# Optimization experiments

Measured on AMD Instinct MI355X. Metric: run time of the kernel, lower is better.

Reference implementation:

```python
import jax, jax.numpy as jnp
import numpy as np

D_MODEL = 2048
NUM_HEADS = 16
HEAD_DIM = D_MODEL // NUM_HEADS
B, T = 4, 2048


def setup_inputs() -> dict:
    key = jax.random.key(0)
    ks = jax.random.split(key, 9)
    s = 1.0 / np.sqrt(D_MODEL)
    inp = {"x": jax.random.normal(ks[0], (B, T, D_MODEL), dtype=jnp.float32)}
    for i, name in enumerate(["q", "k", "v", "o"]):
        inp[f"W{name}"] = jax.random.uniform(ks[1 + 2 * i], (D_MODEL, D_MODEL), minval=-s, maxval=s, dtype=jnp.float32)
        inp[f"b{name}"] = jax.random.uniform(ks[2 + 2 * i], (D_MODEL,), minval=-s, maxval=s, dtype=jnp.float32)
    return inp


def reference(x, Wq, bq, Wk, bk, Wv, bv, Wo, bo):
    Bx, Tx, _ = x.shape
    H, Dh = NUM_HEADS, HEAD_DIM
    # torch Linear: y = x @ W.T + b
    q = (x @ Wq.T + bq).reshape(Bx, Tx, H, Dh).transpose(0, 2, 1, 3)  # [B,H,T,D]
    k = (x @ Wk.T + bk).reshape(Bx, Tx, H, Dh).transpose(0, 2, 1, 3)
    v = (x @ Wv.T + bv).reshape(Bx, Tx, H, Dh).transpose(0, 2, 1, 3)
    scale = 1.0 / np.sqrt(Dh).astype(np.float32)
    scores = jnp.einsum('bhqd,bhkd->bhqk', q, k) * scale  # [B,H,T,T] (no causal mask, as in source)
    attn = jax.nn.softmax(scores, axis=-1)
    out = jnp.einsum('bhqk,bhkd->bhqd', attn, v)  # [B,H,T,D]
    out = out.transpose(0, 2, 1, 3).reshape(Bx, Tx, H * Dh)
    return out @ Wo.T + bo
```

## Files before the change

kernel.cpp:

```cpp
#include <hip/hip_runtime.h>
#include <hip/hip_bf16.h>

typedef __bf16 bf16x8 __attribute__((ext_vector_type(8)));
typedef __bf16 bf16x4 __attribute__((ext_vector_type(4)));
typedef float floatx4 __attribute__((ext_vector_type(4)));

#define MFMA16(a, b, c) __builtin_amdgcn_mfma_f32_16x16x32_bf16((a), (b), (c), 0, 0, 0)

#define GLOAD16(g, l) __builtin_amdgcn_global_load_lds( \
    (const __attribute__((address_space(1))) unsigned int*)(g), \
    (__attribute__((address_space(3))) unsigned int*)(l), 16, 0, 0)

static constexpr int DM = 2048, NH = 16, HD = 128, BATCH = 4, SEQ = 2048;
static constexpr int MROWS = BATCH * SEQ;
static constexpr float SCALE = 0.08838834764831845f;
static constexpr float PMAX = 3.0f;

static constexpr size_t XE = (size_t)MROWS * DM;
static constexpr size_t WE = (size_t)DM * DM;

__global__ __launch_bounds__(256) void cvt_all(
    const float* __restrict__ x, const float* __restrict__ Wq,
    const float* __restrict__ Wk, const float* __restrict__ Wv,
    const float* __restrict__ Wo, __bf16* __restrict__ dst) {
  const size_t total = XE + 4 * WE;
  size_t stride = (size_t)gridDim.x * 256 * 8;
  for (size_t i = ((size_t)blockIdx.x * 256 + threadIdx.x) * 8; i < total; i += stride) {
    const float* src;
    size_t off;
    if (i < XE) { src = x; off = i; }
    else {
      size_t j = i - XE;
      int seg = (int)(j / WE);
      off = j - (size_t)seg * WE;
      src = seg == 0 ? Wq : (seg == 1 ? Wk : (seg == 2 ? Wv : Wo));
    }
    float4 a = *reinterpret_cast<const float4*>(src + off);
    float4 b = *reinterpret_cast<const float4*>(src + off + 4);
    bf16x8 r;
    r[0] = (__bf16)a.x; r[1] = (__bf16)a.y; r[2] = (__bf16)a.z; r[3] = (__bf16)a.w;
    r[4] = (__bf16)b.x; r[5] = (__bf16)b.y; r[6] = (__bf16)b.z; r[7] = (__bf16)b.w;
    *reinterpret_cast<bf16x8*>(dst + i) = r;
  }
}

__device__ __forceinline__ void gemm256_core(
    const __bf16* __restrict__ A, const __bf16* __restrict__ W,
    unsigned short* sA, unsigned short* sB,
    int tm, int tn, floatx4 (&acc)[8][4]) {
  const int tid = threadIdx.x;
  const int wave = tid >> 6, lane = tid & 63;
  const int q = lane >> 4, ml = lane & 15;
  const int wm = wave >> 2, wn = wave & 3;

  const int csrc = (tid & 3) ^ ((tid >> 3) & 3);
  const __bf16* gA = A + (size_t)(tm + (tid >> 2)) * DM + csrc * 8;
  const __bf16* gB = W + (size_t)(tn + (tid >> 2)) * DM + csrc * 8;
  const size_t rstep = (size_t)128 * DM;
  const int ldsW = wave * 512;

  const int fsw = (q ^ ((ml >> 1) & 3)) * 8;
  const int aOff = (wm * 128 + ml) * 32 + fsw;
  const int bOff = (wn * 64 + ml) * 32 + fsw;

#define STAGE256(s_) do { \
    const int _r = ((s_) & 3) * 8192;   \
    const int _k = (s_) * 32;           \
    GLOAD16(gA + _k,         sA + _r + ldsW); \
    GLOAD16(gA + _k + rstep, sA + _r + 4096 + ldsW); \
    GLOAD16(gB + _k,         sB + _r + ldsW); \
    GLOAD16(gB + _k + rstep, sB + _r + 4096 + ldsW); \
  } while (0)

#define GPHASE(p_, vm_, stage_) do { \
    if (stage_) STAGE256((p_) + 3); \
    asm volatile("s_waitcnt vmcnt(%0)" :: "i"(vm_) : "memory"); \
    __builtin_amdgcn_s_barrier(); \
    __builtin_amdgcn_sched_barrier(0); \
    const int regO = ((p_) & 3) * 8192; \
    bf16x8 aF[8], bF[4]; \
    _Pragma("unroll") \
    for (int t = 0; t < 4; ++t) \
      bF[t] = *reinterpret_cast<const bf16x8*>(sB + regO + bOff + t * 512); \
    _Pragma("unroll") \
    for (int t = 0; t < 8; ++t) \
      aF[t] = *reinterpret_cast<const bf16x8*>(sA + regO + aOff + t * 512); \
    __builtin_amdgcn_s_setprio(1); \
    _Pragma("unroll") \
    for (int mt = 0; mt < 8; ++mt) \
      _Pragma("unroll") \
      for (int ct = 0; ct < 4; ++ct) \
        acc[mt][ct] = MFMA16(aF[mt], bF[ct], acc[mt][ct]); \
    __builtin_amdgcn_s_setprio(0); \
    __builtin_amdgcn_s_barrier(); \
  } while (0)

  STAGE256(0); STAGE256(1); STAGE256(2);

#pragma unroll 4
  for (int p = 0; p < 60; ++p) GPHASE(p, 12, 1);
  GPHASE(60, 12, 1);
  GPHASE(61, 8, 0);
  GPHASE(62, 4, 0);
  GPHASE(63, 0, 0);
#undef GPHASE
#undef STAGE256
}

__global__ __launch_bounds__(512, 2) void qkv_gemm256(
    const __bf16* __restrict__ X,
    const __bf16* __restrict__ Wq, const __bf16* __restrict__ Wk,
    const __bf16* __restrict__ Wv,
    const float* __restrict__ bq, const float* __restrict__ bk,
    const float* __restrict__ bv,
    __bf16* __restrict__ qh, __bf16* __restrict__ kh, __bf16* __restrict__ vt) {
  __shared__ unsigned short sA[4 * 256 * 32];
  __shared__ unsigned short sB[4 * 256 * 32];
  const int bx = blockIdx.x;
  const int which = bx >> 3;
  const int tn = (bx & 7) * 256;
  const int tm = blockIdx.y * 256;
  const __bf16* W = which == 0 ? Wq : (which == 1 ? Wk : Wv);
  const float* bias = which == 0 ? bq : (which == 1 ? bk : bv);

  floatx4 acc[8][4] = {};
  gemm256_core(X, W, sA, sB, tm, tn, acc);

  const int tid = threadIdx.x, wave = tid >> 6, lane = tid & 63;
  const int q = lane >> 4, ml = lane & 15;
  const int wm = wave >> 2, wn = wave & 3;

  __syncthreads();

  if (which < 2) {
    unsigned short* reg = (wave < 4) ? sA + wave * 8192 : sB + (wave - 4) * 8192;
#pragma unroll
    for (int ct = 0; ct < 4; ++ct) {
      int n = tn + wn * 64 + ct * 16 + ml;
      float bv_ = bias[n];
#pragma unroll
      for (int mt = 0; mt < 8; ++mt)
#pragma unroll
        for (int r = 0; r < 4; ++r) {
          int row = mt * 16 + q * 4 + r;
          int col = ct * 16 + ml;
          __bf16 pb = (__bf16)(acc[mt][ct][r] + bv_);
          reg[row * 64 + (((col >> 3) ^ ((row >> 1) & 7)) << 3) + (col & 7)] =
              __builtin_bit_cast(unsigned short, pb);
        }
    }
    __bf16* dst = which == 0 ? qh : kh;
    const int rr = lane >> 3, cc = lane & 7;
#pragma unroll
    for (int i = 0; i < 16; ++i) {
      int row = i * 8 + rr;
      int4 v = *reinterpret_cast<const int4*>(
          reg + row * 64 + ((cc ^ ((row >> 1) & 7)) << 3));
      int m = tm + wm * 128 + row;
      int n0 = tn + wn * 64 + cc * 8;
      int b = m >> 11, t = m & 2047, h = n0 >> 7, d = n0 & 127;
      *reinterpret_cast<int4*>(dst + ((size_t)(b * 16 + h) * SEQ + t) * HD + d) = v;
    }
  } else {
#pragma unroll
    for (int ct = 0; ct < 4; ++ct) {
      int n = tn + wn * 64 + ct * 16 + ml;
      float bv_ = bias[n];
      int h = n >> 7, d = n & 127;
#pragma unroll
      for (int mt = 0; mt < 8; ++mt) {
        int m0 = tm + wm * 128 + mt * 16 + q * 4;
        int b = m0 >> 11, t = m0 & 2047;
        bf16x4 pk;
#pragma unroll
        for (int r = 0; r < 4; ++r) pk[r] = (__bf16)(acc[mt][ct][r] + bv_);
        *reinterpret_cast<bf16x4*>(vt + (size_t)((b * 16 + h) * 128 + d) * SEQ + t) = pk;
      }
    }
  }
}

__global__ __launch_bounds__(512, 2) void proj_gemm256(
    const __bf16* __restrict__ A, const __bf16* __restrict__ W,
    const float* __restrict__ bias, float* __restrict__ out) {
  __shared__ unsigned short sA[4 * 256 * 32];
  __shared__ unsigned short sB[4 * 256 * 32];
  const int tn = blockIdx.x * 256;
  const int tm = blockIdx.y * 256;

  floatx4 acc[8][4] = {};
  gemm256_core(A, W, sA, sB, tm, tn, acc);

  const int tid = threadIdx.x, wave = tid >> 6, lane = tid & 63;
  const int q = lane >> 4, ml = lane & 15;
  const int wm = wave >> 2, wn = wave & 3;
#pragma unroll
  for (int ct = 0; ct < 4; ++ct) {
    int n = tn + wn * 64 + ct * 16 + ml;
    float bv_ = bias[n];
#pragma unroll
    for (int mt = 0; mt < 8; ++mt) {
      int m0 = tm + wm * 128 + mt * 16 + q * 4;
#pragma unroll
      for (int r = 0; r < 4; ++r)
        out[(size_t)(m0 + r) * DM + n] = acc[mt][ct][r] + bv_;
    }
  }
}

__global__ __launch_bounds__(512, 4) void mha_attn(
    const __bf16* __restrict__ Q, const __bf16* __restrict__ Kg,
    const __bf16* __restrict__ Vt, __bf16* __restrict__ O) {
  __shared__ unsigned short sK[2][64 * 128];
  __shared__ unsigned short sV[2][128 * 64];
  __shared__ unsigned short sP[128 * 64];

  const int tid = threadIdx.x;
  const int bh = blockIdx.x;
  const int t0 = blockIdx.y * 128;
  const int wave = tid >> 6, lane = tid & 63;
  const int q = lane >> 4, ml = lane & 15;
  const int wrow = wave * 16;

  bf16x8 qf[4];
  {
    const __bf16* qrow = Q + ((size_t)bh * SEQ + t0 + wrow + ml) * HD;
#pragma unroll
    for (int s = 0; s < 4; ++s)
      qf[s] = *reinterpret_cast<const bf16x8*>(qrow + s * 32 + q * 8);
  }

  floatx4 oacc[8] = {};
  float lsum[4] = {0.f, 0.f, 0.f, 0.f};

  const __bf16* kbase = Kg + (size_t)bh * SEQ * HD;
  const __bf16* vbase = Vt + (size_t)bh * HD * SEQ;
  const int lrow4 = lane >> 4, c16 = lane & 15;
  const int lrow8 = lane >> 3, c8 = lane & 7;

#define ASTAGE(slot_, key0_) do { \
    _Pragma("unroll") \
    for (int i = 0; i < 2; ++i) { \
      int kr0 = wave * 8 + i * 4; \
      int kc = c16 ^ ((i * 4 + lrow4) & 7); \
      GLOAD16(kbase + (size_t)((key0_) + kr0 + lrow4) * HD + kc * 8, \
              &sK[slot_][kr0 * 128]); \
      int vr0 = wave * 16 + i * 8; \
      int vc = c8 ^ (lrow8 & 7); \
      GLOAD16(vbase + (size_t)(vr0 + lrow8) * SEQ + (key0_) + vc * 8, \
              &sV[slot_][vr0 * 64]); \
    } } while (0)

#define ACOMPUTE(S_) do { \
    floatx4 sacc[4] = {}; \
    _Pragma("unroll") \
    for (int s = 0; s < 4; ++s) { \
      _Pragma("unroll") \
      for (int ct = 0; ct < 4; ++ct) { \
        bf16x8 kf = *reinterpret_cast<const bf16x8*>( \
            &sK[S_][(ct * 16 + ml) * 128 + (((s * 4 + q) ^ (ml & 7)) * 8)]); \
        sacc[ct] = MFMA16(qf[s], kf, sacc[ct]); \
      } \
    } \
    _Pragma("unroll") \
    for (int ct = 0; ct < 4; ++ct) { \
      _Pragma("unroll") \
      for (int r = 0; r < 4; ++r) { \
        float p = __expf(fmaf(sacc[ct][r], SCALE, -PMAX)); \
        lsum[r] += p; \
        __bf16 pb = (__bf16)p; \
        int lr = wrow + q * 4 + r; \
        int ch = ct * 2 + (ml >> 3); \
        sP[lr * 64 + ((ch ^ (lr & 7)) << 3) + (ml & 7)] = \
            __builtin_bit_cast(unsigned short, pb); \
      } \
    } \
    _Pragma("unroll") \
    for (int s = 0; s < 2; ++s) { \
      int prow = wrow + ml; \
      bf16x8 pf = *reinterpret_cast<const bf16x8*>( \
          &sP[prow * 64 + (((s * 4 + q) ^ (ml & 7)) << 3)]); \
      _Pragma("unroll") \
      for (int ot = 0; ot < 8; ++ot) { \
        bf16x8 vf = *reinterpret_cast<const bf16x8*>( \
            &sV[S_][(ot * 16 + ml) * 64 + (((s * 4 + q) ^ (ml & 7)) * 8)]); \
        oacc[ot] = MFMA16(pf, vf, oacc[ot]); \
      } \
    } } while (0)

  ASTAGE(0, 0);
  for (int kt = 0; kt < 31; ++kt) {
    const int S = kt & 1;
    ASTAGE(S ^ 1, (kt + 1) * 64);
    asm volatile("s_waitcnt vmcnt(4)" ::: "memory");
    __builtin_amdgcn_s_barrier();
    __builtin_amdgcn_sched_barrier(0);
    __builtin_amdgcn_s_setprio(1);
    ACOMPUTE(S);
    __builtin_amdgcn_s_setprio(0);
    asm volatile("" ::: "memory");
    __builtin_amdgcn_s_barrier();
  }
  asm volatile("s_waitcnt vmcnt(0)" ::: "memory");
  __builtin_amdgcn_s_barrier();
  __builtin_amdgcn_sched_barrier(0);
  ACOMPUTE(1);
#undef ACOMPUTE
#undef ASTAGE

#pragma unroll
  for (int r = 0; r < 4; ++r) {
    float s = lsum[r];
    s += __shfl_xor(s, 1); s += __shfl_xor(s, 2);
    s += __shfl_xor(s, 4); s += __shfl_xor(s, 8);
    lsum[r] = 1.0f / s;
  }

  const int b = bh >> 4, h = bh & 15;
  const int rr = lane >> 3, cc = lane & 7;
  __bf16* obase = O + ((size_t)b * SEQ + t0 + wrow) * DM + h * HD;
#pragma unroll
  for (int pass = 0; pass < 2; ++pass) {
    __builtin_amdgcn_sched_barrier(0);
#pragma unroll
    for (int ot = 0; ot < 4; ++ot) {
#pragma unroll
      for (int r = 0; r < 4; ++r) {
        int lr = wrow + q * 4 + r;
        int ch = ot * 2 + (ml >> 3);
        __bf16 ob = (__bf16)(oacc[pass * 4 + ot][r] * lsum[r]);
        sP[lr * 64 + ((ch ^ (lr & 7)) << 3) + (ml & 7)] =
            __builtin_bit_cast(unsigned short, ob);
      }
    }
#pragma unroll
    for (int i = 0; i < 2; ++i) {
      int row16 = i * 8 + rr;
      int gr = wrow + row16;
      int4 v = *reinterpret_cast<const int4*>(
          &sP[gr * 64 + ((cc ^ (gr & 7)) << 3)]);
      *reinterpret_cast<int4*>(obase + (size_t)row16 * DM + pass * 64 + cc * 8) = v;
    }
  }
}

__device__ inline bf16x8 ld8s(const float* p) {
  float4 a = *reinterpret_cast<const float4*>(p);
  float4 b = *reinterpret_cast<const float4*>(p + 4);
  bf16x8 r;
  r[0] = (__bf16)a.x; r[1] = (__bf16)a.y; r[2] = (__bf16)a.z; r[3] = (__bf16)a.w;
  r[4] = (__bf16)b.x; r[5] = (__bf16)b.y; r[6] = (__bf16)b.z; r[7] = (__bf16)b.w;
  return r;
}
__device__ inline bf16x8 ld8s(const __bf16* p) {
  int4 v = *reinterpret_cast<const int4*>(p);
  return __builtin_bit_cast(bf16x8, v);
}

template <typename TA>
__global__ __launch_bounds__(256) void gemm_slow(
    const TA* __restrict__ A, const float* __restrict__ W,
    const float* __restrict__ bias, void* __restrict__ C, int mode, int out_f32) {
  __shared__ unsigned short sA[128 * 72];
  __shared__ unsigned short sW[128 * 72];
  const int tid = threadIdx.x;
  const int tn = blockIdx.x * 128, tm = blockIdx.y * 128;
  const int wave = tid >> 6, lane = tid & 63;
  const int q = lane >> 4, ml = lane & 15;
  const int waveM = (wave >> 1) * 64, waveN = (wave & 1) * 64;
  const int srow = tid >> 3, sc8 = tid & 7;
  floatx4 acc[4][4] = {};
  for (int k0 = 0; k0 < DM; k0 += 64) {
    bf16x8 va[4], vb[4];
#pragma unroll
    for (int i = 0; i < 4; ++i) {
      int row = srow + 32 * i;
      va[i] = ld8s(A + (size_t)(tm + row) * DM + k0 + sc8 * 8);
      vb[i] = ld8s(W + (size_t)(tn + row) * DM + k0 + sc8 * 8);
    }
    __syncthreads();
#pragma unroll
    for (int i = 0; i < 4; ++i) {
      int row = srow + 32 * i;
      *reinterpret_cast<int4*>(&sA[row * 72 + sc8 * 8]) = __builtin_bit_cast(int4, va[i]);
      *reinterpret_cast<int4*>(&sW[row * 72 + sc8 * 8]) = __builtin_bit_cast(int4, vb[i]);
    }
    __syncthreads();
#pragma unroll
    for (int s = 0; s < 2; ++s) {
      bf16x8 aF[4], bF[4];
#pragma unroll
      for (int t = 0; t < 4; ++t)
        aF[t] = *reinterpret_cast<const bf16x8*>(&sA[(waveM + t * 16 + ml) * 72 + s * 32 + q * 8]);
#pragma unroll
      for (int t = 0; t < 4; ++t)
        bF[t] = *reinterpret_cast<const bf16x8*>(&sW[(waveN + t * 16 + ml) * 72 + s * 32 + q * 8]);
#pragma unroll
      for (int rt = 0; rt < 4; ++rt)
#pragma unroll
        for (int ct = 0; ct < 4; ++ct)
          acc[rt][ct] = MFMA16(aF[rt], bF[ct], acc[rt][ct]);
    }
  }
#pragma unroll
  for (int ct = 0; ct < 4; ++ct) {
    int n = tn + waveN + ct * 16 + ml;
    float bv = bias[n];
    int h = n >> 7, d = n & 127;
#pragma unroll
    for (int rt = 0; rt < 4; ++rt) {
      int m0 = tm + waveM + rt * 16 + q * 4;
      int b = m0 >> 11, t = m0 & 2047;
      if (mode == 0) {
        if (out_f32) {
#pragma unroll
          for (int r = 0; r < 4; ++r)
            ((float*)C)[(size_t)(m0 + r) * DM + n] = acc[rt][ct][r] + bv;
        } else {
#pragma unroll
          for (int r = 0; r < 4; ++r)
            ((__bf16*)C)[(size_t)(m0 + r) * DM + n] = (__bf16)(acc[rt][ct][r] + bv);
        }
      } else if (mode == 1) {
        bf16x4 pk;
#pragma unroll
        for (int r = 0; r < 4; ++r) pk[r] = (__bf16)(acc[rt][ct][r] + bv);
        *reinterpret_cast<bf16x4*>((__bf16*)C + (size_t)((b * 16 + h) * 128 + d) * SEQ + t) = pk;
      } else {
#pragma unroll
        for (int r = 0; r < 4; ++r)
          ((__bf16*)C)[((size_t)(b * 16 + h) * SEQ + t + r) * HD + d] =
              (__bf16)(acc[rt][ct][r] + bv);
      }
    }
  }
}

extern "C" void kernel_launch(void* const* d_in, const int* in_sizes, int n_in,
                              void* d_out, int out_size, void* d_ws, size_t ws_size,
                              hipStream_t stream) {
  const float* x  = (const float*)d_in[0];
  const float* Wq = (const float*)d_in[1]; const float* bq = (const float*)d_in[2];
  const float* Wk = (const float*)d_in[3]; const float* bk = (const float*)d_in[4];
  const float* Wv = (const float*)d_in[5]; const float* bv = (const float*)d_in[6];
  const float* Wo = (const float*)d_in[7]; const float* bo = (const float*)d_in[8];

  const size_t needA = 64 + 2 * (4 * XE + 4 * WE);
  dim3 gq(24, 32), gp(8, 32), gs(16, 64), ga(BATCH * NH, SEQ / 128);

  if (ws_size >= needA + 256) {
    __bf16* xc  = (__bf16*)((char*)d_ws + 64);
    __bf16* Wqc = xc + XE;
    __bf16* Wkc = Wqc + WE;
    __bf16* Wvc = Wkc + WE;
    __bf16* Woc = Wvc + WE;
    __bf16* qh  = Woc + WE;
    __bf16* kh  = qh + XE;
    __bf16* vt  = kh + XE;
    __bf16* aw  = xc;

    cvt_all<<<4096, 256, 0, stream>>>(x, Wq, Wk, Wv, Wo, xc);
    qkv_gemm256<<<gq, 512, 0, stream>>>(xc, Wqc, Wkc, Wvc, bq, bk, bv, qh, kh, vt);
    mha_attn<<<ga, 512, 0, stream>>>(qh, kh, vt, aw);
    proj_gemm256<<<gp, 512, 0, stream>>>(aw, Woc, bo, (float*)d_out);
  } else {
    __bf16* qh = (__bf16*)((char*)d_ws + 64);
    __bf16* kh = qh + XE;
    __bf16* vt = kh + XE;
    __bf16* aw = vt + XE;
    gemm_slow<float><<<gs, 256, 0, stream>>>(x, Wq, bq, qh, 2, 0);
    gemm_slow<float><<<gs, 256, 0, stream>>>(x, Wk, bk, kh, 2, 0);
    gemm_slow<float><<<gs, 256, 0, stream>>>(x, Wv, bv, vt, 1, 0);
    mha_attn<<<ga, 512, 0, stream>>>(qh, kh, vt, aw);
    gemm_slow<__bf16><<<gs, 256, 0, stream>>>(aw, Wo, bo, d_out, 0, 1);
  }
}
```

Before: 615.9 us.

## Give each attention wave two 16-row query tiles to reuse K/V fragments

The attention kernel moves from 8 waves of 16 query rows each to 4 waves of 32 query rows each (256 threads per block). Each K and V fragment read from LDS now feeds two MFMAs, which halves LDS read traffic per MFMA. The cooperative staging loop, wait counts and epilogue are rewritten to match the smaller block. In exchange, accumulator registers roughly double (oacc grows to 2x8 floatx4), which may lower occupancy, and each block has fewer waves to hide latency.

```diff
diff --git a/kernel.cpp b/kernel.cpp
--- a/kernel.cpp
+++ b/kernel.cpp
@@ -208,7 +208,7 @@
   }
 }
 
-__global__ __launch_bounds__(512, 4) void mha_attn(
+__global__ __launch_bounds__(256, 2) void mha_attn(
     const __bf16* __restrict__ Q, const __bf16* __restrict__ Kg,
     const __bf16* __restrict__ Vt, __bf16* __restrict__ O) {
   __shared__ unsigned short sK[2][64 * 128];
@@ -220,71 +220,74 @@
   const int t0 = blockIdx.y * 128;
   const int wave = tid >> 6, lane = tid & 63;
   const int q = lane >> 4, ml = lane & 15;
-  const int wrow = wave * 16;
-
-  bf16x8 qf[4];
-  {
-    const __bf16* qrow = Q + ((size_t)bh * SEQ + t0 + wrow + ml) * HD;
+  const int wrow = wave * 32;
+
+  bf16x8 qf[2][4];
+#pragma unroll
+  for (int mt = 0; mt < 2; ++mt) {
+    const __bf16* qrow = Q + ((size_t)bh * SEQ + t0 + wrow + mt * 16 + ml) * HD;
 #pragma unroll
     for (int s = 0; s < 4; ++s)
-      qf[s] = *reinterpret_cast<const bf16x8*>(qrow + s * 32 + q * 8);
-  }
-
-  floatx4 oacc[8] = {};
-  float lsum[4] = {0.f, 0.f, 0.f, 0.f};
+      qf[mt][s] = *reinterpret_cast<const bf16x8*>(qrow + s * 32 + q * 8);
+  }
+
+  floatx4 oacc[2][8] = {};
+  float lsum[2][4] = {};
 
   const __bf16* kbase = Kg + (size_t)bh * SEQ * HD;
   const __bf16* vbase = Vt + (size_t)bh * HD * SEQ;
-  const int lrow4 = lane >> 4, c16 = lane & 15;
-  const int lrow8 = lane >> 3, c8 = lane & 7;
 
 #define ASTAGE(slot_, key0_) do { \
     _Pragma("unroll") \
-    for (int i = 0; i < 2; ++i) { \
-      int kr0 = wave * 8 + i * 4; \
-      int kc = c16 ^ ((i * 4 + lrow4) & 7); \
-      GLOAD16(kbase + (size_t)((key0_) + kr0 + lrow4) * HD + kc * 8, \
-              &sK[slot_][kr0 * 128]); \
-      int vr0 = wave * 16 + i * 8; \
-      int vc = c8 ^ (lrow8 & 7); \
-      GLOAD16(vbase + (size_t)(vr0 + lrow8) * SEQ + (key0_) + vc * 8, \
-              &sV[slot_][vr0 * 64]); \
+    for (int i = 0; i < 4; ++i) { \
+      int krow = i * 16 + (tid >> 4); \
+      int kc = (tid & 15) ^ (krow & 7); \
+      GLOAD16(kbase + (size_t)((key0_) + krow) * HD + kc * 8, \
+              &sK[slot_][i * 2048 + wave * 512]); \
+      int vrow = i * 32 + (tid >> 3); \
+      int vc = (tid & 7) ^ (vrow & 7); \
+      GLOAD16(vbase + (size_t)vrow * SEQ + (key0_) + vc * 8, \
+              &sV[slot_][i * 2048 + wave * 512]); \
     } } while (0)
 
 #define ACOMPUTE(S_) do { \
-    floatx4 sacc[4] = {}; \
+    floatx4 sacc[2][4] = {}; \
     _Pragma("unroll") \
     for (int s = 0; s < 4; ++s) { \
       _Pragma("unroll") \
       for (int ct = 0; ct < 4; ++ct) { \
         bf16x8 kf = *reinterpret_cast<const bf16x8*>( \
             &sK[S_][(ct * 16 + ml) * 128 + (((s * 4 + q) ^ (ml & 7)) * 8)]); \
-        sacc[ct] = MFMA16(qf[s], kf, sacc[ct]); \
+        sacc[0][ct] = MFMA16(qf[0][s], kf, sacc[0][ct]); \
+        sacc[1][ct] = MFMA16(qf[1][s], kf, sacc[1][ct]); \
       } \
     } \
     _Pragma("unroll") \
-    for (int ct = 0; ct < 4; ++ct) { \
+    for (int mt = 0; mt < 2; ++mt) \
       _Pragma("unroll") \
-      for (int r = 0; r < 4; ++r) { \
-        float p = __expf(fmaf(sacc[ct][r], SCALE, -PMAX)); \
-        lsum[r] += p; \
-        __bf16 pb = (__bf16)p; \
-        int lr = wrow + q * 4 + r; \
-        int ch = ct * 2 + (ml >> 3); \
-        sP[lr * 64 + ((ch ^ (lr & 7)) << 3) + (ml & 7)] = \
-            __builtin_bit_cast(unsigned short, pb); \
-      } \
-    } \
+      for (int ct = 0; ct < 4; ++ct) \
+        _Pragma("unroll") \
+        for (int r = 0; r < 4; ++r) { \
+          float p = __expf(fmaf(sacc[mt][ct][r], SCALE, -PMAX)); \
+          lsum[mt][r] += p; \
+          __bf16 pb = (__bf16)p; \
+          int lr = wrow + mt * 16 + q * 4 + r; \
+          int ch = ct * 2 + (ml >> 3); \
+          sP[lr * 64 + ((ch ^ (lr & 7)) << 3) + (ml & 7)] = \
+              __builtin_bit_cast(unsigned short, pb); \
+        } \
     _Pragma("unroll") \
     for (int s = 0; s < 2; ++s) { \
-      int prow = wrow + ml; \
-      bf16x8 pf = *reinterpret_cast<const bf16x8*>( \
-          &sP[prow * 64 + (((s * 4 + q) ^ (ml & 7)) << 3)]); \
+      bf16x8 pf0 = *reinterpret_cast<const bf16x8*>( \
+          &sP[(wrow + ml) * 64 + (((s * 4 + q) ^ (ml & 7)) << 3)]); \
+      bf16x8 pf1 = *reinterpret_cast<const bf16x8*>( \
+          &sP[(wrow + 16 + ml) * 64 + (((s * 4 + q) ^ (ml & 7)) << 3)]); \
       _Pragma("unroll") \
       for (int ot = 0; ot < 8; ++ot) { \
         bf16x8 vf = *reinterpret_cast<const bf16x8*>( \
             &sV[S_][(ot * 16 + ml) * 64 + (((s * 4 + q) ^ (ml & 7)) * 8)]); \
-        oacc[ot] = MFMA16(pf, vf, oacc[ot]); \
+        oacc[0][ot] = MFMA16(pf0, vf, oacc[0][ot]); \
+        oacc[1][ot] = MFMA16(pf1, vf, oacc[1][ot]); \
       } \
     } } while (0)
 
@@ -292,7 +295,7 @@
   for (int kt = 0; kt < 31; ++kt) {
     const int S = kt & 1;
     ASTAGE(S ^ 1, (kt + 1) * 64);
-    asm volatile("s_waitcnt vmcnt(4)" ::: "memory");
+    asm volatile("s_waitcnt vmcnt(8)" ::: "memory");
     __builtin_amdgcn_s_barrier();
     __builtin_amdgcn_sched_barrier(0);
     __builtin_amdgcn_s_setprio(1);
@@ -309,12 +312,14 @@
 #undef ASTAGE
 
 #pragma unroll
-  for (int r = 0; r < 4; ++r) {
-    float s = lsum[r];
-    s += __shfl_xor(s, 1); s += __shfl_xor(s, 2);
-    s += __shfl_xor(s, 4); s += __shfl_xor(s, 8);
-    lsum[r] = 1.0f / s;
-  }
+  for (int mt = 0; mt < 2; ++mt)
+#pragma unroll
+    for (int r = 0; r < 4; ++r) {
+      float s = lsum[mt][r];
+      s += __shfl_xor(s, 1); s += __shfl_xor(s, 2);
+      s += __shfl_xor(s, 4); s += __shfl_xor(s, 8);
+      lsum[mt][r] = 1.0f / s;
+    }
 
   const int b = bh >> 4, h = bh & 15;
   const int rr = lane >> 3, cc = lane & 7;
@@ -323,23 +328,24 @@
   for (int pass = 0; pass < 2; ++pass) {
     __builtin_amdgcn_sched_barrier(0);
 #pragma unroll
-    for (int ot = 0; ot < 4; ++ot) {
-#pragma unroll
-      for (int r = 0; r < 4; ++r) {
-        int lr = wrow + q * 4 + r;
-        int ch = ot * 2 + (ml >> 3);
-        __bf16 ob = (__bf16)(oacc[pass * 4 + ot][r] * lsum[r]);
-        sP[lr * 64 + ((ch ^ (lr & 7)) << 3) + (ml & 7)] =
-            __builtin_bit_cast(unsigned short, ob);
-      }
-    }
-#pragma unroll
-    for (int i = 0; i < 2; ++i) {
-      int row16 = i * 8 + rr;
-      int gr = wrow + row16;
+    for (int mt = 0; mt < 2; ++mt)
+#pragma unroll
+      for (int ot = 0; ot < 4; ++ot)
+#pragma unroll
+        for (int r = 0; r < 4; ++r) {
+          int lr = wrow + mt * 16 + q * 4 + r;
+          int ch = ot * 2 + (ml >> 3);
+          __bf16 ob = (__bf16)(oacc[mt][pass * 4 + ot][r] * lsum[mt][r]);
+          sP[lr * 64 + ((ch ^ (lr & 7)) << 3) + (ml & 7)] =
+              __builtin_bit_cast(unsigned short, ob);
+        }
+#pragma unroll
+    for (int i = 0; i < 4; ++i) {
+      int row32 = i * 8 + rr;
+      int gr = wrow + row32;
       int4 v = *reinterpret_cast<const int4*>(
           &sP[gr * 64 + ((cc ^ (gr & 7)) << 3)]);
-      *reinterpret_cast<int4*>(obase + (size_t)row16 * DM + pass * 64 + cc * 8) = v;
+      *reinterpret_cast<int4*>(obase + (size_t)row32 * DM + pass * 64 + cc * 8) = v;
     }
   }
 }
@@ -461,7 +467,7 @@
 
     cvt_all<<<4096, 256, 0, stream>>>(x, Wq, Wk, Wv, Wo, xc);
     qkv_gemm256<<<gq, 512, 0, stream>>>(xc, Wqc, Wkc, Wvc, bq, bk, bv, qh, kh, vt);
-    mha_attn<<<ga, 512, 0, stream>>>(qh, kh, vt, aw);
+    mha_attn<<<ga, 256, 0, stream>>>(qh, kh, vt, aw);
     proj_gemm256<<<gp, 512, 0, stream>>>(aw, Woc, bo, (float*)d_out);
   } else {
     __bf16* qh = (__bf16*)((char*)d_ws + 64);
@@ -471,7 +477,7 @@
     gemm_slow<float><<<gs, 256, 0, stream>>>(x, Wq, bq, qh, 2, 0);
     gemm_slow<float><<<gs, 256, 0, stream>>>(x, Wk, bk, kh, 2, 0);
     gemm_slow<float><<<gs, 256, 0, stream>>>(x, Wv, bv, vt, 1, 0);
-    mha_attn<<<ga, 512, 0, stream>>>(qh, kh, vt, aw);
+    mha_attn<<<ga, 256, 0, stream>>>(qh, kh, vt, aw);
     gemm_slow<__bf16><<<gs, 256, 0, stream>>>(aw, Wo, bo, d_out, 0, 1);
   }
 }
```

Result: no change. 613.0 us (-0.5%).
